# Performance work log

Hardware: AMD Instinct MI355X
Metric: run time of the kernel (lower is better)

The kernel has to match this reference:

```python
import jax, jax.numpy as jnp
import numpy as np

B = 8
H_IN, W_IN = 448, 448
STRIDE = 32
NUM_CLASSES = 20
CONF_THRESH = 0.01
NMS_THRESH = 0.5
HS, WS = H_IN // STRIDE, W_IN // STRIDE  # 14, 14
N_CELLS = HS * WS  # 196
CHANNELS = [3, 64, 128, 256, 512, 512]
HEAD_OUT = 1 + NUM_CLASSES + 4  # 25


def _conv(x, w, stride):
    return jax.lax.conv_general_dilated(
        x, w, (stride, stride), 'SAME',
        dimension_numbers=('NCHW', 'OIHW', 'NCHW'))


def _create_grid():
    gy, gx = jnp.meshgrid(jnp.arange(HS), jnp.arange(WS), indexing='ij')
    return jnp.stack([gx, gy], -1).reshape(1, N_CELLS, 2).astype(jnp.float32)


def _iou_matrix(boxes):
    # boxes: [N,4] xyxy -> [N,N] pairwise IoU
    x1, y1, x2, y2 = boxes[:, 0], boxes[:, 1], boxes[:, 2], boxes[:, 3]
    area = jnp.maximum(x2 - x1, 0.0) * jnp.maximum(y2 - y1, 0.0)
    ix1 = jnp.maximum(x1[:, None], x1[None, :])
    iy1 = jnp.maximum(y1[:, None], y1[None, :])
    ix2 = jnp.minimum(x2[:, None], x2[None, :])
    iy2 = jnp.minimum(y2[:, None], y2[None, :])
    inter = jnp.maximum(ix2 - ix1, 0.0) * jnp.maximum(iy2 - iy1, 0.0)
    return inter / (area[:, None] + area[None, :] - inter + 1e-14)


def _nms_keep(scores, iou):
    # greedy per-class NMS; scores [N], iou [N,N] -> bool keep mask [N]
    order = jnp.argsort(-scores)
    iou_s = iou[order][:, order]
    idx = jnp.arange(N_CELLS)
    valid = scores[order] > CONF_THRESH

    def body(i, keep):
        sup = (iou_s[i] > NMS_THRESH) & (idx > i) & keep[i]
        return keep & (~sup)

    keep = jax.lax.fori_loop(0, N_CELLS, body, valid)
    return jnp.zeros(N_CELLS, bool).at[order].set(keep)


def setup_inputs() -> dict:
    key = jax.random.key(0)
    ks = jax.random.split(key, 8)
    x = jax.random.normal(ks[0], (B, 3, H_IN, W_IN), dtype=jnp.float32)
    params = {}
    for i in range(5):
        cin, cout = CHANNELS[i], CHANNELS[i + 1]
        std = np.sqrt(2.0 / (cin * 9))
        params[f'w{i+1}'] = jax.random.normal(ks[i + 1], (cout, cin, 3, 3), dtype=jnp.float32) * std
    std = np.sqrt(2.0 / CHANNELS[-1])
    params['w_head'] = jax.random.normal(ks[6], (HEAD_OUT, CHANNELS[-1], 1, 1), dtype=jnp.float32) * std
    return {'x': x, **params}


def reference(x, w1, w2, w3, w4, w5, w_head):
    # backbone: 5 stride-2 conv+relu stages -> stride 32
    h = x
    for w in (w1, w2, w3, w4, w5):
        h = jax.nn.relu(_conv(h, w, 2))
    pred = _conv(h, w_head, 1)                      # [B, 25, 14, 14]
    pred = pred.reshape(B, HEAD_OUT, N_CELLS).transpose(0, 2, 1)  # [B, N, 25]

    conf = jax.nn.sigmoid(pred[..., 0:1])                              # [B,N,1]
    cls_scores = jax.nn.softmax(pred[..., 1:1 + NUM_CLASSES], -1) * conf  # [B,N,C]
    txtytwth = pred[..., 1 + NUM_CLASSES:]                             # [B,N,4]

    grid = _create_grid()                                              # [1,N,2]
    xy = (jax.nn.sigmoid(txtytwth[..., :2]) + grid) * STRIDE
    wh = jnp.exp(txtytwth[..., 2:]) * STRIDE
    scale = jnp.array([W_IN, H_IN, W_IN, H_IN], dtype=jnp.float32)
    boxes = jnp.concatenate([xy - wh * 0.5, xy + wh * 0.5], -1) / scale
    boxes = jnp.clip(boxes, 0.0, 1.0)                                  # [B,N,4]

    iou = jax.vmap(_iou_matrix)(boxes)                                 # [B,N,N]
    # per-class NMS, vmapped over classes then batch
    nms_c = jax.vmap(_nms_keep, in_axes=(-1, None), out_axes=-1)       # [N,C]
    keep = jax.vmap(nms_c, in_axes=(0, 0))(cls_scores, iou)            # [B,N,C]
    final_scores = cls_scores * keep
    return jnp.concatenate([boxes, final_scores], -1)                  # [B,N,4+C]
```

## Files before the change

### kernel.cpp

```cpp
#include <hip/hip_runtime.h>
#include <math.h>

#define BATCH 8
#define NCELLS 196
#define NCLS 20
#define HEADC 25

typedef __attribute__((ext_vector_type(8))) short short8;
typedef __attribute__((ext_vector_type(4))) float f32x4;
#define MFMA16(a,b,c) __builtin_amdgcn_mfma_f32_16x16x32_bf16(a,b,c,0,0,0)

__device__ __forceinline__ unsigned short f2bf(float x) {
    union { float f; unsigned u; } a; a.f = x;
    unsigned r = a.u + 0x7FFFu + ((a.u >> 16) & 1u);
    return (unsigned short)(r >> 16);
}
__device__ __forceinline__ float bf2f(unsigned short h) {
    union { unsigned u; float f; } a; a.u = ((unsigned)h) << 16;
    return a.f;
}
__device__ __forceinline__ void split_bf(float x, unsigned short& h, unsigned short& l) {
    h = f2bf(x);
    l = f2bf(x - bf2f(h));
}

__device__ __forceinline__ void prep_one(const float* __restrict__ w, int CIN, int COUT,
                                         int idx, unsigned short* __restrict__ whi,
                                         unsigned short* __restrict__ wlo) {
    int G = COUT >> 4, CH = CIN >> 5;
    int j    = idx & 7;
    int lane = (idx >> 3) & 63;
    int fg   = idx >> 9;
    int g    = fg % G;
    int fc   = fg / G;
    int chunk = fc % CH;
    int plane = fc / CH;
    int co = g * 16 + (lane & 15);
    int ci = chunk * 32 + (lane >> 4) * 8 + j;
    int ky = plane / 3, kx = plane % 3;
    float v = w[((co * CIN + ci) * 3 + ky) * 3 + kx];
    unsigned short h, l; split_bf(v, h, l);
    whi[idx] = h; wlo[idx] = l;
}
__global__ void prep_all(const float* __restrict__ w2, const float* __restrict__ w3,
                         const float* __restrict__ w4, const float* __restrict__ w5,
                         unsigned short* __restrict__ w2h, unsigned short* __restrict__ w2l,
                         unsigned short* __restrict__ w3h, unsigned short* __restrict__ w3l,
                         unsigned short* __restrict__ w4h, unsigned short* __restrict__ w4l,
                         unsigned short* __restrict__ w5h, unsigned short* __restrict__ w5l) {
    int idx = blockIdx.x * 256 + threadIdx.x;
    const int n2 = 73728, n3 = 294912, n4 = 1179648, n5 = 2359296;
    if (idx < n2) { prep_one(w2, 64, 128, idx, w2h, w2l); return; }
    idx -= n2;
    if (idx < n3) { prep_one(w3, 128, 256, idx, w3h, w3l); return; }
    idx -= n3;
    if (idx < n4) { prep_one(w4, 256, 512, idx, w4h, w4l); return; }
    idx -= n4;
    if (idx < n5) { prep_one(w5, 512, 512, idx, w5h, w5l); }
}

__global__ void conv1_kernel(const float* __restrict__ x, const float* __restrict__ w1,
                             unsigned short* __restrict__ ohi, unsigned short* __restrict__ olo) {
    __shared__ float sW[27][64];
    __shared__ float sX[3][3][66];
    int bid = blockIdx.x;
    int xseg = bid % 7;  bid /= 7;
    int oy   = bid % 224;
    int b    = bid / 224;
    int ox0  = xseg * 32;

    for (int e = threadIdx.x; e < 1728; e += 256) {
        int k = e >> 6, co = e & 63;
        sW[k][co] = w1[co * 27 + k];
    }
    for (int e = threadIdx.x; e < 594; e += 256) {
        int ci = e / 198;
        int r  = e - ci * 198;
        int ky = r / 66;
        int lx = r - ky * 66;
        int iy = 2 * oy + ky;
        int ix = 2 * ox0 + lx;
        float v = 0.f;
        if (lx < 65 && iy < 448 && ix < 448)
            v = x[(((size_t)b * 3 + ci) * 448 + iy) * 448 + ix];
        sX[ci][ky][lx] = v;
    }
    __syncthreads();

    int pxl = threadIdx.x >> 3;
    int cog = threadIdx.x & 7;
    float acc[8] = {0.f,0.f,0.f,0.f,0.f,0.f,0.f,0.f};
    #pragma unroll
    for (int ci = 0; ci < 3; ci++) {
        #pragma unroll
        for (int ky = 0; ky < 3; ky++) {
            const float* row = sX[ci][ky];
            #pragma unroll
            for (int kx = 0; kx < 3; kx++) {
                float iv = row[2 * pxl + kx];
                int k = (ci * 3 + ky) * 3 + kx;
                float4 wa = *(const float4*)&sW[k][cog * 8];
                float4 wb = *(const float4*)&sW[k][cog * 8 + 4];
                acc[0] += wa.x * iv; acc[1] += wa.y * iv; acc[2] += wa.z * iv; acc[3] += wa.w * iv;
                acc[4] += wb.x * iv; acc[5] += wb.y * iv; acc[6] += wb.z * iv; acc[7] += wb.w * iv;
            }
        }
    }
    union { unsigned short u[8]; uint4 v; } ph, pl;
    #pragma unroll
    for (int u = 0; u < 8; u++) {
        float v = fmaxf(acc[u], 0.f);
        split_bf(v, ph.u[u], pl.u[u]);
    }
    size_t base = ((size_t)(b * 224 + oy) * 224 + ox0 + pxl) * 64 + cog * 8;
    *(uint4*)&ohi[base] = ph.v;
    *(uint4*)&olo[base] = pl.v;
}

template<int CIN, int COUT, int HIN, int WIN, int KSPLIT, bool PARTIAL>
__launch_bounds__(256, 4)
__global__ void conv_mfma(const unsigned short* __restrict__ ahi, const unsigned short* __restrict__ alo,
                          const unsigned short* __restrict__ whi, const unsigned short* __restrict__ wlo,
                          unsigned short* __restrict__ ohi, unsigned short* __restrict__ olo,
                          float* __restrict__ part) {
    constexpr int HOUT = HIN / 2, WOUT = WIN / 2;
    constexpr int TX = (WOUT + 7) / 8, TY = (HOUT + 7) / 8;
    constexpr int COG = COUT / 128;
    constexpr int CH_TOT = CIN / 32;
    constexpr int CH = CH_TOT / KSPLIT;
    constexpr int G = COUT / 16;
    constexpr int PLANE_E = 17 * 17 * 32;
    constexpr size_t PSZ = (size_t)BATCH * HOUT * WOUT * COUT;

    __shared__ __align__(16) unsigned short sA[2 * PLANE_E];

    int bid = blockIdx.x;
    int ks  = bid % KSPLIT; bid /= KSPLIT;
    int txi = bid % TX;     bid /= TX;
    int tyi = bid % TY;     bid /= TY;
    int cg  = bid % COG;
    int b   = bid / COG;
    int oy0 = tyi * 8, ox0 = txi * 8;
    int iy0 = oy0 * 2, ix0 = ox0 * 2;

    int tid = threadIdx.x;
    int w   = tid >> 6;
    int lane = tid & 63;
    int n = lane & 15, quad = lane >> 4;
    int cohalf = w & 1;
    int pxhalf = w >> 1;

    int oyl[2], oxl[2], pbase[2];
    #pragma unroll
    for (int t = 0; t < 2; t++) {
        int nt = pxhalf * 2 + t;
        int oy_off = (nt >> 1) * 4 + (n >> 2);
        int ox_off = (nt & 1) * 4 + (n & 3);
        oyl[t] = oy0 + oy_off;
        oxl[t] = ox0 + ox_off;
        pbase[t] = 2 * oy_off * 17 + 2 * ox_off;
    }

    f32x4 zero = {0.f, 0.f, 0.f, 0.f};
    f32x4 acc[4][2];
    #pragma unroll
    for (int g = 0; g < 4; g++)
        #pragma unroll
        for (int t = 0; t < 2; t++) acc[g][t] = zero;

    int g0 = cg * 8 + cohalf * 4;

    for (int ch = 0; ch < CH; ch++) {
        int chunk = ks * CH + ch;
        int ci0 = chunk * 32;
        __syncthreads();
        for (int e = tid; e < 17 * 17 * 8; e += 256) {
            int pxi = e >> 3, grp = e & 7;
            int liy = pxi / 17, lix = pxi - liy * 17;
            int iy = iy0 + liy, ix = ix0 + lix;
            uint4 v = make_uint4(0u, 0u, 0u, 0u);
            if (iy < HIN && ix < WIN) {
                const unsigned short* src = ((grp & 4) ? alo : ahi)
                    + ((size_t)(b * HIN + iy) * WIN + ix) * CIN + ci0 + (grp & 3) * 8;
                v = *(const uint4*)src;
            }
            int u = pxi * 4 + ((grp & 3) ^ ((pxi >> 1) & 3));
            *(uint4*)&sA[((grp >> 2) ? PLANE_E : 0) + u * 8] = v;
        }
        __syncthreads();
        #pragma unroll
        for (int pl = 0; pl < 9; pl++) {
            int ky = pl / 3, kx = pl % 3;
            size_t fbase = ((size_t)(pl * CH_TOT + chunk) * G + g0) * 512 + lane * 8;
            short8 Ah[4], Al[4];
            #pragma unroll
            for (int g = 0; g < 4; g++) {
                Ah[g] = *(const short8*)(whi + fbase + (size_t)g * 512);
                Al[g] = *(const short8*)(wlo + fbase + (size_t)g * 512);
            }
            int dp = ky * 17 + kx;
            short8 Bh[2], Bl[2];
            #pragma unroll
            for (int t = 0; t < 2; t++) {
                int p = pbase[t] + dp;
                int u = p * 4 + (quad ^ ((p >> 1) & 3));
                Bh[t] = *(const short8*)&sA[u * 8];
                Bl[t] = *(const short8*)&sA[PLANE_E + u * 8];
            }
            #pragma unroll
            for (int g = 0; g < 4; g++) {
                #pragma unroll
                for (int t = 0; t < 2; t++) {
                    acc[g][t] = MFMA16(Ah[g], Bh[t], acc[g][t]);
                    acc[g][t] = MFMA16(Ah[g], Bl[t], acc[g][t]);
                    acc[g][t] = MFMA16(Al[g], Bh[t], acc[g][t]);
                }
            }
        }
    }
    int cob = cg * 128 + cohalf * 64;
    #pragma unroll
    for (int g = 0; g < 4; g++) {
        #pragma unroll
        for (int t = 0; t < 2; t++) {
            if (oyl[t] >= HOUT || oxl[t] >= WOUT) continue;
            size_t base = ((size_t)(b * HOUT + oyl[t]) * WOUT + oxl[t]) * COUT
                          + cob + g * 16 + quad * 4;
            if (PARTIAL) {
                *(f32x4*)&part[(size_t)ks * PSZ + base] = acc[g][t];
            } else {
                unsigned long long h64 = 0ull, l64 = 0ull;
                #pragma unroll
                for (int r = 0; r < 4; r++) {
                    float v = fmaxf(acc[g][t][r], 0.f);
                    unsigned short hh, ll; split_bf(v, hh, ll);
                    h64 |= ((unsigned long long)hh) << (16 * r);
                    l64 |= ((unsigned long long)ll) << (16 * r);
                }
                *(unsigned long long*)&ohi[base] = h64;
                *(unsigned long long*)&olo[base] = l64;
            }
        }
    }
}

template<int KS>
__global__ void reduceN_split(const float* __restrict__ p, unsigned short* __restrict__ oh,
                              unsigned short* __restrict__ ol, int n) {
    int n4 = n >> 2;
    int i = blockIdx.x * 256 + threadIdx.x;
    if (i >= n4) return;
    const float4* p4 = (const float4*)p;
    float4 s = p4[i];
    #pragma unroll
    for (int k = 1; k < KS; k++) {
        float4 t = p4[i + (size_t)k * n4];
        s.x += t.x; s.y += t.y; s.z += t.z; s.w += t.w;
    }
    float v[4] = { fmaxf(s.x,0.f), fmaxf(s.y,0.f), fmaxf(s.z,0.f), fmaxf(s.w,0.f) };
    unsigned long long h64 = 0ull, l64 = 0ull;
    #pragma unroll
    for (int r = 0; r < 4; r++) {
        unsigned short hh, ll; split_bf(v[r], hh, ll);
        h64 |= ((unsigned long long)hh) << (16 * r);
        l64 |= ((unsigned long long)ll) << (16 * r);
    }
    *(unsigned long long*)&oh[i * 4] = h64;
    *(unsigned long long*)&ol[i * 4] = l64;
}

__global__ void head_decode_kernel(const unsigned short* __restrict__ ah,
                                   const unsigned short* __restrict__ al,
                                   const float* __restrict__ wh,
                                   float* __restrict__ out, float* __restrict__ cls) {
    int wave = threadIdx.x >> 6;
    int lane = threadIdx.x & 63;
    int cellid = blockIdx.x * 4 + wave;
    float acc[HEADC];
    #pragma unroll
    for (int c = 0; c < HEADC; c++) acc[c] = 0.f;
    for (int it = 0; it < 8; it++) {
        int ci = it * 64 + lane;
        size_t idx = (size_t)cellid * 512 + ci;
        float a = bf2f(ah[idx]) + bf2f(al[idx]);
        #pragma unroll
        for (int c = 0; c < HEADC; c++) acc[c] += a * wh[c * 512 + ci];
    }
    #pragma unroll
    for (int c = 0; c < HEADC; c++) {
        float v = acc[c];
        v += __shfl_down(v, 32); v += __shfl_down(v, 16); v += __shfl_down(v, 8);
        v += __shfl_down(v, 4);  v += __shfl_down(v, 2);  v += __shfl_down(v, 1);
        acc[c] = v;
    }
    if (lane == 0) {
        int cell = cellid % NCELLS;
        int gx = cell % 14, gy = cell / 14;
        float conf = 1.f / (1.f + expf(-acc[0]));
        float m = acc[1];
        #pragma unroll
        for (int c = 1; c < NCLS; c++) m = fmaxf(m, acc[1 + c]);
        float e[NCLS], s = 0.f;
        #pragma unroll
        for (int c = 0; c < NCLS; c++) { e[c] = expf(acc[1 + c] - m); s += e[c]; }
        float inv = conf / s;
        #pragma unroll
        for (int c = 0; c < NCLS; c++) cls[(size_t)cellid * NCLS + c] = e[c] * inv;
        float cx = (1.f / (1.f + expf(-acc[21])) + gx) * 32.f;
        float cy = (1.f / (1.f + expf(-acc[22])) + gy) * 32.f;
        float bw = expf(acc[23]) * 32.f;
        float bh = expf(acc[24]) * 32.f;
        float x1 = (cx - 0.5f * bw) / 448.f, y1 = (cy - 0.5f * bh) / 448.f;
        float x2 = (cx + 0.5f * bw) / 448.f, y2 = (cy + 0.5f * bh) / 448.f;
        x1 = fminf(fmaxf(x1, 0.f), 1.f); y1 = fminf(fmaxf(y1, 0.f), 1.f);
        x2 = fminf(fmaxf(x2, 0.f), 1.f); y2 = fminf(fmaxf(y2, 0.f), 1.f);
        float* o = out + (size_t)cellid * 24;
        o[0] = x1; o[1] = y1; o[2] = x2; o[3] = y2;
    }
}

__global__ void iou_kernel(const float* __restrict__ out, float* __restrict__ iou) {
    int idx = blockIdx.x * 256 + threadIdx.x;
    if (idx >= BATCH * NCELLS * NCELLS) return;
    int j = idx % NCELLS;
    int i = (idx / NCELLS) % NCELLS;
    int b = idx / (NCELLS * NCELLS);
    const float* bi = out + (((size_t)b * NCELLS) + i) * 24;
    const float* bj = out + (((size_t)b * NCELLS) + j) * 24;
    float ai = fmaxf(bi[2] - bi[0], 0.f) * fmaxf(bi[3] - bi[1], 0.f);
    float aj = fmaxf(bj[2] - bj[0], 0.f) * fmaxf(bj[3] - bj[1], 0.f);
    float ix1 = fmaxf(bi[0], bj[0]), iy1 = fmaxf(bi[1], bj[1]);
    float ix2 = fminf(bi[2], bj[2]), iy2 = fminf(bi[3], bj[3]);
    float inter = fmaxf(ix2 - ix1, 0.f) * fmaxf(iy2 - iy1, 0.f);
    iou[idx] = inter / (ai + aj - inter + 1e-14f);
}

__global__ void nms_kernel(const float* __restrict__ cls, const float* __restrict__ iou,
                           float* __restrict__ out) {
    int b = blockIdx.x / NCLS;
    int c = blockIdx.x % NCLS;
    __shared__ float sc[NCELLS];
    __shared__ float ssort[NCELLS];
    __shared__ int   ord[NCELLS];
    __shared__ __align__(16) unsigned long long smask[NCELLS][4];
    int j = threadIdx.x;
    int lane = j & 63;
    int w = j >> 6;
    float sj = 0.f;
    if (j < NCELLS) {
        sj = cls[(((size_t)b * NCELLS) + j) * NCLS + c];
        sc[j] = sj;
    }
    __syncthreads();
    if (j < NCELLS) {
        int r = 0;
        for (int k = 0; k < NCELLS; k++) {
            float sk = sc[k];
            r += (sk > sj) || (sk == sj && k < j);
        }
        ord[r] = j; ssort[r] = sj;
    }
    __syncthreads();
    const float* iob = iou + (size_t)b * NCELLS * NCELLS;
    int oc[4];
    #pragma unroll
    for (int k = 0; k < 4; k++) {
        int cidx = k * 64 + lane;
        oc[k] = (cidx < NCELLS) ? ord[cidx] : 0;
    }
    for (int i = w; i < NCELLS; i += 4) {
        const float* rowp = iob + ord[i] * NCELLS;
        #pragma unroll
        for (int k = 0; k < 4; k++) {
            int cidx = k * 64 + lane;
            bool sup = false;
            if (cidx < NCELLS && cidx > i)
                sup = rowp[oc[k]] > 0.5f;
            unsigned long long m = __ballot(sup);
            if (lane == 0) smask[i][k] = m;
        }
    }
    __syncthreads();
    unsigned long long keep[4];
    #pragma unroll
    for (int k = 0; k < 4; k++) {
        int cidx = k * 64 + lane;
        bool valid = (cidx < NCELLS) && (ssort[cidx] > 0.01f);
        keep[k] = __ballot(valid);
    }
    #pragma unroll
    for (int wi = 0; wi < 4; wi++) {
        int base = wi * 64;
        int lim = (NCELLS - base < 64) ? (NCELLS - base) : 64;
        for (int t = 0; t < lim; t++) {
            if ((keep[wi] >> t) & 1ull) {
                int i = base + t;
                keep[0] &= ~smask[i][0];
                keep[1] &= ~smask[i][1];
                keep[2] &= ~smask[i][2];
                keep[3] &= ~smask[i][3];
            }
        }
    }
    if (j < NCELLS) {
        bool kept = (keep[w] >> lane) & 1ull;
        out[(((size_t)b * NCELLS) + ord[j]) * 24 + 4 + c] = kept ? ssort[j] : 0.f;
    }
}

extern "C" void kernel_launch(void* const* d_in, const int* in_sizes, int n_in,
                              void* d_out, int out_size, void* d_ws, size_t ws_size,
                              hipStream_t stream) {
    const float* x  = (const float*)d_in[0];
    const float* w1 = (const float*)d_in[1];
    const float* w2 = (const float*)d_in[2];
    const float* w3 = (const float*)d_in[3];
    const float* w4 = (const float*)d_in[4];
    const float* w5 = (const float*)d_in[5];
    const float* wh = (const float*)d_in[6];
    float* out = (float*)d_out;
    char* base = (char*)d_ws;

    unsigned short* a1h = (unsigned short*)(base);
    unsigned short* a1l = a1h + 25690112;
    unsigned short* a3h = (unsigned short*)(base);
    unsigned short* a3l = a3h + 6422528;
    float* part4 = (float*)(base + 25690112);
    float* part5 = (float*)(base);
    unsigned short* a5h = (unsigned short*)(base + 51380224);
    unsigned short* a5l = a5h + 802816;
    float* clsb = (float*)(base + 54746240);
    float* ioub = (float*)(base + 54871680);
    unsigned short* a2h = (unsigned short*)(base + 102760448);
    unsigned short* a2l = a2h + 12845056;
    unsigned short* a4h = (unsigned short*)(base + 102760448);
    unsigned short* a4l = a4h + 3211264;
    unsigned short* w2h = (unsigned short*)(base + 154140672);
    unsigned short* w3h = w2h + 73728;
    unsigned short* w4h = w3h + 294912;
    unsigned short* w5h = w4h + 1179648;
    unsigned short* w2l = (unsigned short*)(base + 161955840);
    unsigned short* w3l = w2l + 73728;
    unsigned short* w4l = w3l + 294912;
    unsigned short* w5l = w4l + 1179648;

    prep_all<<<15264, 256, 0, stream>>>(w2, w3, w4, w5,
                                        w2h, w2l, w3h, w3l, w4h, w4l, w5h, w5l);

    conv1_kernel<<<12544, 256, 0, stream>>>(x, w1, a1h, a1l);

    conv_mfma<64, 128, 224, 224, 1, false><<<1568, 256, 0, stream>>>(
        a1h, a1l, w2h, w2l, a2h, a2l, nullptr);
    conv_mfma<128, 256, 112, 112, 1, false><<<784, 256, 0, stream>>>(
        a2h, a2l, w3h, w3l, a3h, a3l, nullptr);
    conv_mfma<256, 512, 56, 56, 2, true><<<1024, 256, 0, stream>>>(
        a3h, a3l, w4h, w4l, nullptr, nullptr, part4);
    reduceN_split<2><<<3136, 256, 0, stream>>>(part4, a4h, a4l, 3211264);
    conv_mfma<512, 512, 28, 28, 8, true><<<1024, 256, 0, stream>>>(
        a4h, a4l, w5h, w5l, nullptr, nullptr, part5);
    reduceN_split<8><<<784, 256, 0, stream>>>(part5, a5h, a5l, 802816);

    head_decode_kernel<<<392, 256, 0, stream>>>(a5h, a5l, wh, out, clsb);
    iou_kernel<<<1201, 256, 0, stream>>>(out, ioub);
    nms_kernel<<<160, 256, 0, stream>>>(clsb, ioub, out);
}
```

Baseline: 464.2 us.

## Double-buffer conv input tiles in LDS using async global-to-LDS loads

Replaces the synchronous register-staged copy of each 32-channel input chunk into shared memory with direct global-to-LDS loads (global_load_lds), double-buffered so the next chunk is fetched while MFMAs run on the current one. The swizzle moves to the source address side, and out-of-bounds slots are zero-filled with ordinary stores. Only one barrier per chunk remains instead of two. Shared memory per block doubles and launch bounds drop from 4 to 2 blocks per CU, which trades occupancy for overlap.

```diff
diff --git a/kernel.cpp b/kernel.cpp
--- a/kernel.cpp
+++ b/kernel.cpp
@@ -9,6 +9,10 @@
 typedef __attribute__((ext_vector_type(8))) short short8;
 typedef __attribute__((ext_vector_type(4))) float f32x4;
 #define MFMA16(a,b,c) __builtin_amdgcn_mfma_f32_16x16x32_bf16(a,b,c,0,0,0)
+
+#define GLOAD_LDS16(g, l) \
+    __builtin_amdgcn_global_load_lds((const __attribute__((address_space(1))) void*)(g), \
+                                     (__attribute__((address_space(3))) void*)(l), 16, 0, 0)
 
 __device__ __forceinline__ unsigned short f2bf(float x) {
     union { float f; unsigned u; } a; a.f = x;
@@ -118,7 +122,7 @@
 }
 
 template<int CIN, int COUT, int HIN, int WIN, int KSPLIT, bool PARTIAL>
-__launch_bounds__(256, 4)
+__launch_bounds__(256, 2)
 __global__ void conv_mfma(const unsigned short* __restrict__ ahi, const unsigned short* __restrict__ alo,
                           const unsigned short* __restrict__ whi, const unsigned short* __restrict__ wlo,
                           unsigned short* __restrict__ ohi, unsigned short* __restrict__ olo,
@@ -129,10 +133,10 @@
     constexpr int CH_TOT = CIN / 32;
     constexpr int CH = CH_TOT / KSPLIT;
     constexpr int G = COUT / 16;
-    constexpr int PLANE_E = 17 * 17 * 32;
+    constexpr int UNITS = 17 * 17 * 4;
     constexpr size_t PSZ = (size_t)BATCH * HOUT * WOUT * COUT;
 
-    __shared__ __align__(16) unsigned short sA[2 * PLANE_E];
+    __shared__ __align__(16) unsigned short sA[2][2][UNITS * 8];
 
     int bid = blockIdx.x;
     int ks  = bid % KSPLIT; bid /= KSPLIT;
@@ -170,27 +174,38 @@
 
     int g0 = cg * 8 + cohalf * 4;
 
+    auto stage = [&](int ch, int buf) {
+        int ci0 = (ks * CH + ch) * 32;
+        #pragma unroll
+        for (int m = 0; m < (UNITS + 255) / 256; m++) {
+            int e = m * 256 + tid;
+            if (e < UNITS) {
+                int pxi = e >> 2, gsl = e & 3;
+                int grp = gsl ^ ((pxi >> 1) & 3);
+                int liy = pxi / 17, lix = pxi - liy * 17;
+                int iy = iy0 + liy, ix = ix0 + lix;
+                if (iy < HIN && ix < WIN) {
+                    size_t off = ((size_t)(b * HIN + iy) * WIN + ix) * CIN + ci0 + grp * 8;
+                    int ebase = m * 256 + (tid & 192);
+                    GLOAD_LDS16(ahi + off, &sA[buf][0][ebase * 8]);
+                    GLOAD_LDS16(alo + off, &sA[buf][1][ebase * 8]);
+                } else {
+                    uint4 z = make_uint4(0u, 0u, 0u, 0u);
+                    *(uint4*)&sA[buf][0][e * 8] = z;
+                    *(uint4*)&sA[buf][1][e * 8] = z;
+                }
+            }
+        }
+    };
+
+    stage(0, 0);
+    int pb = 0;
     for (int ch = 0; ch < CH; ch++) {
+        __syncthreads();
+        if (ch + 1 < CH) stage(ch + 1, pb ^ 1);
         int chunk = ks * CH + ch;
-        int ci0 = chunk * 32;
-        __syncthreads();
-        for (int e = tid; e < 17 * 17 * 8; e += 256) {
-            int pxi = e >> 3, grp = e & 7;
-            int liy = pxi / 17, lix = pxi - liy * 17;
-            int iy = iy0 + liy, ix = ix0 + lix;
-            uint4 v = make_uint4(0u, 0u, 0u, 0u);
-            if (iy < HIN && ix < WIN) {
-                const unsigned short* src = ((grp & 4) ? alo : ahi)
-                    + ((size_t)(b * HIN + iy) * WIN + ix) * CIN + ci0 + (grp & 3) * 8;
-                v = *(const uint4*)src;
-            }
-            int u = pxi * 4 + ((grp & 3) ^ ((pxi >> 1) & 3));
-            *(uint4*)&sA[((grp >> 2) ? PLANE_E : 0) + u * 8] = v;
-        }
-        __syncthreads();
         #pragma unroll
         for (int pl = 0; pl < 9; pl++) {
-            int ky = pl / 3, kx = pl % 3;
             size_t fbase = ((size_t)(pl * CH_TOT + chunk) * G + g0) * 512 + lane * 8;
             short8 Ah[4], Al[4];
             #pragma unroll
@@ -198,14 +213,14 @@
                 Ah[g] = *(const short8*)(whi + fbase + (size_t)g * 512);
                 Al[g] = *(const short8*)(wlo + fbase + (size_t)g * 512);
             }
-            int dp = ky * 17 + kx;
+            int dp = (pl / 3) * 17 + (pl % 3);
             short8 Bh[2], Bl[2];
             #pragma unroll
             for (int t = 0; t < 2; t++) {
                 int p = pbase[t] + dp;
                 int u = p * 4 + (quad ^ ((p >> 1) & 3));
-                Bh[t] = *(const short8*)&sA[u * 8];
-                Bl[t] = *(const short8*)&sA[PLANE_E + u * 8];
+                Bh[t] = *(const short8*)&sA[pb][0][u * 8];
+                Bl[t] = *(const short8*)&sA[pb][1][u * 8];
             }
             #pragma unroll
             for (int g = 0; g < 4; g++) {
@@ -217,7 +232,9 @@
                 }
             }
         }
-    }
+        pb ^= 1;
+    }
+
     int cob = cg * 128 + cohalf * 64;
     #pragma unroll
     for (int g = 0; g < 4; g++) {
```

After: 487.8 us. +5.1%, slower.

## Retile conv MFMA warps with prefetched weights; fuse IoU into NMS

Applied to the files above, without the earlier changes.

The conv MFMA kernel now gives each warp 2 output-channel groups across all 4 pixel tiles, instead of 4 groups across 2 tiles. This changes the mix of weight loads and LDS activation loads per warp. It also adds a 3-slot register prefetch of weight fragments so global loads overlap the MFMAs. Separately, the standalone IoU kernel and its global N×N matrix are removed, and NMS computes IoU on the fly from boxes staged in shared memory. This saves a launch and the IoU matrix traffic but repeats the IoU arithmetic for every class block.

```diff
diff --git a/kernel.cpp b/kernel.cpp
--- a/kernel.cpp
+++ b/kernel.cpp
@@ -147,28 +147,26 @@
     int w   = tid >> 6;
     int lane = tid & 63;
     int n = lane & 15, quad = lane >> 4;
-    int cohalf = w & 1;
-    int pxhalf = w >> 1;
-
-    int oyl[2], oxl[2], pbase[2];
-    #pragma unroll
-    for (int t = 0; t < 2; t++) {
-        int nt = pxhalf * 2 + t;
-        int oy_off = (nt >> 1) * 4 + (n >> 2);
-        int ox_off = (nt & 1) * 4 + (n & 3);
-        oyl[t] = oy0 + oy_off;
-        oxl[t] = ox0 + ox_off;
-        pbase[t] = 2 * oy_off * 17 + 2 * ox_off;
+
+    int oyl[4], oxl[4], pbase[4];
+    #pragma unroll
+    for (int nt = 0; nt < 4; nt++) {
+        int oyq = nt >> 1, oxq = nt & 1;
+        int oy_off = oyq * 4 + (n >> 2);
+        int ox_off = oxq * 4 + (n & 3);
+        oyl[nt] = oy0 + oy_off;
+        oxl[nt] = ox0 + ox_off;
+        pbase[nt] = 2 * oy_off * 17 + 2 * ox_off;
     }
 
     f32x4 zero = {0.f, 0.f, 0.f, 0.f};
-    f32x4 acc[4][2];
-    #pragma unroll
-    for (int g = 0; g < 4; g++)
-        #pragma unroll
-        for (int t = 0; t < 2; t++) acc[g][t] = zero;
-
-    int g0 = cg * 8 + cohalf * 4;
+    f32x4 acc[2][4];
+    #pragma unroll
+    for (int ct = 0; ct < 2; ct++)
+        #pragma unroll
+        for (int nt = 0; nt < 4; nt++) acc[ct][nt] = zero;
+
+    int g0 = cg * 8 + w * 2;
 
     for (int ch = 0; ch < CH; ch++) {
         int chunk = ks * CH + ch;
@@ -188,51 +186,50 @@
             *(uint4*)&sA[((grp >> 2) ? PLANE_E : 0) + u * 8] = v;
         }
         __syncthreads();
+        short8 Ah[3][2], Al[3][2];
+        auto loadA = [&](int pl, int slot) {
+            size_t fbase = ((size_t)(pl * CH_TOT + chunk) * G + g0) * 512 + lane * 8;
+            Ah[slot][0] = *(const short8*)(whi + fbase);
+            Ah[slot][1] = *(const short8*)(whi + fbase + 512);
+            Al[slot][0] = *(const short8*)(wlo + fbase);
+            Al[slot][1] = *(const short8*)(wlo + fbase + 512);
+        };
+        loadA(0, 0); loadA(1, 1); loadA(2, 2);
         #pragma unroll
         for (int pl = 0; pl < 9; pl++) {
-            int ky = pl / 3, kx = pl % 3;
-            size_t fbase = ((size_t)(pl * CH_TOT + chunk) * G + g0) * 512 + lane * 8;
-            short8 Ah[4], Al[4];
+            const int slot = pl % 3;
+            int dp = (pl / 3) * 17 + (pl % 3);
             #pragma unroll
-            for (int g = 0; g < 4; g++) {
-                Ah[g] = *(const short8*)(whi + fbase + (size_t)g * 512);
-                Al[g] = *(const short8*)(wlo + fbase + (size_t)g * 512);
-            }
-            int dp = ky * 17 + kx;
-            short8 Bh[2], Bl[2];
-            #pragma unroll
-            for (int t = 0; t < 2; t++) {
-                int p = pbase[t] + dp;
+            for (int nt = 0; nt < 4; nt++) {
+                int p = pbase[nt] + dp;
                 int u = p * 4 + (quad ^ ((p >> 1) & 3));
-                Bh[t] = *(const short8*)&sA[u * 8];
-                Bl[t] = *(const short8*)&sA[PLANE_E + u * 8];
-            }
-            #pragma unroll
-            for (int g = 0; g < 4; g++) {
-                #pragma unroll
-                for (int t = 0; t < 2; t++) {
-                    acc[g][t] = MFMA16(Ah[g], Bh[t], acc[g][t]);
-                    acc[g][t] = MFMA16(Ah[g], Bl[t], acc[g][t]);
-                    acc[g][t] = MFMA16(Al[g], Bh[t], acc[g][t]);
-                }
-            }
-        }
-    }
-    int cob = cg * 128 + cohalf * 64;
-    #pragma unroll
-    for (int g = 0; g < 4; g++) {
-        #pragma unroll
-        for (int t = 0; t < 2; t++) {
-            if (oyl[t] >= HOUT || oxl[t] >= WOUT) continue;
-            size_t base = ((size_t)(b * HOUT + oyl[t]) * WOUT + oxl[t]) * COUT
-                          + cob + g * 16 + quad * 4;
+                short8 Bh = *(const short8*)&sA[u * 8];
+                short8 Bl = *(const short8*)&sA[PLANE_E + u * 8];
+                acc[0][nt] = MFMA16(Ah[slot][0], Bh, acc[0][nt]);
+                acc[0][nt] = MFMA16(Ah[slot][0], Bl, acc[0][nt]);
+                acc[0][nt] = MFMA16(Al[slot][0], Bh, acc[0][nt]);
+                acc[1][nt] = MFMA16(Ah[slot][1], Bh, acc[1][nt]);
+                acc[1][nt] = MFMA16(Ah[slot][1], Bl, acc[1][nt]);
+                acc[1][nt] = MFMA16(Al[slot][1], Bh, acc[1][nt]);
+            }
+            if (pl + 3 < 9) loadA(pl + 3, slot);
+        }
+    }
+    int cob = cg * 128 + w * 32;
+    #pragma unroll
+    for (int ct = 0; ct < 2; ct++) {
+        #pragma unroll
+        for (int nt = 0; nt < 4; nt++) {
+            if (oyl[nt] >= HOUT || oxl[nt] >= WOUT) continue;
+            size_t base = ((size_t)(b * HOUT + oyl[nt]) * WOUT + oxl[nt]) * COUT
+                          + cob + ct * 16 + quad * 4;
             if (PARTIAL) {
-                *(f32x4*)&part[(size_t)ks * PSZ + base] = acc[g][t];
+                *(f32x4*)&part[(size_t)ks * PSZ + base] = acc[ct][nt];
             } else {
                 unsigned long long h64 = 0ull, l64 = 0ull;
                 #pragma unroll
                 for (int r = 0; r < 4; r++) {
-                    float v = fmaxf(acc[g][t][r], 0.f);
+                    float v = fmaxf(acc[ct][nt][r], 0.f);
                     unsigned short hh, ll; split_bf(v, hh, ll);
                     h64 |= ((unsigned long long)hh) << (16 * r);
                     l64 |= ((unsigned long long)ll) << (16 * r);
@@ -319,29 +316,15 @@
     }
 }
 
-__global__ void iou_kernel(const float* __restrict__ out, float* __restrict__ iou) {
-    int idx = blockIdx.x * 256 + threadIdx.x;
-    if (idx >= BATCH * NCELLS * NCELLS) return;
-    int j = idx % NCELLS;
-    int i = (idx / NCELLS) % NCELLS;
-    int b = idx / (NCELLS * NCELLS);
-    const float* bi = out + (((size_t)b * NCELLS) + i) * 24;
-    const float* bj = out + (((size_t)b * NCELLS) + j) * 24;
-    float ai = fmaxf(bi[2] - bi[0], 0.f) * fmaxf(bi[3] - bi[1], 0.f);
-    float aj = fmaxf(bj[2] - bj[0], 0.f) * fmaxf(bj[3] - bj[1], 0.f);
-    float ix1 = fmaxf(bi[0], bj[0]), iy1 = fmaxf(bi[1], bj[1]);
-    float ix2 = fminf(bi[2], bj[2]), iy2 = fminf(bi[3], bj[3]);
-    float inter = fmaxf(ix2 - ix1, 0.f) * fmaxf(iy2 - iy1, 0.f);
-    iou[idx] = inter / (ai + aj - inter + 1e-14f);
-}
-
-__global__ void nms_kernel(const float* __restrict__ cls, const float* __restrict__ iou,
+__global__ void nms_kernel(const float* __restrict__ cls, const float* __restrict__ boxes,
                            float* __restrict__ out) {
     int b = blockIdx.x / NCLS;
     int c = blockIdx.x % NCLS;
     __shared__ float sc[NCELLS];
     __shared__ float ssort[NCELLS];
     __shared__ int   ord[NCELLS];
+    __shared__ __align__(16) float sbox[NCELLS][4];
+    __shared__ float sarea[NCELLS];
     __shared__ __align__(16) unsigned long long smask[NCELLS][4];
     int j = threadIdx.x;
     int lane = j & 63;
@@ -350,6 +333,9 @@
     if (j < NCELLS) {
         sj = cls[(((size_t)b * NCELLS) + j) * NCLS + c];
         sc[j] = sj;
+        float4 bx = *(const float4*)&boxes[(((size_t)b * NCELLS) + j) * 24];
+        *(float4*)sbox[j] = bx;
+        sarea[j] = fmaxf(bx.z - bx.x, 0.f) * fmaxf(bx.w - bx.y, 0.f);
     }
     __syncthreads();
     if (j < NCELLS) {
@@ -361,21 +347,31 @@
         ord[r] = j; ssort[r] = sj;
     }
     __syncthreads();
-    const float* iob = iou + (size_t)b * NCELLS * NCELLS;
-    int oc[4];
+    int oc[4]; float bx1[4], by1[4], bx2[4], by2[4], bar[4];
     #pragma unroll
     for (int k = 0; k < 4; k++) {
         int cidx = k * 64 + lane;
         oc[k] = (cidx < NCELLS) ? ord[cidx] : 0;
+        bx1[k] = sbox[oc[k]][0]; by1[k] = sbox[oc[k]][1];
+        bx2[k] = sbox[oc[k]][2]; by2[k] = sbox[oc[k]][3];
+        bar[k] = sarea[oc[k]];
     }
     for (int i = w; i < NCELLS; i += 4) {
-        const float* rowp = iob + ord[i] * NCELLS;
+        int oi = ord[i];
+        float ix1 = sbox[oi][0], iy1 = sbox[oi][1];
+        float ix2 = sbox[oi][2], iy2 = sbox[oi][3];
+        float ia  = sarea[oi];
         #pragma unroll
         for (int k = 0; k < 4; k++) {
             int cidx = k * 64 + lane;
             bool sup = false;
-            if (cidx < NCELLS && cidx > i)
-                sup = rowp[oc[k]] > 0.5f;
+            if (cidx < NCELLS && cidx > i) {
+                float xx1 = fmaxf(ix1, bx1[k]), yy1 = fmaxf(iy1, by1[k]);
+                float xx2 = fminf(ix2, bx2[k]), yy2 = fminf(iy2, by2[k]);
+                float inter = fmaxf(xx2 - xx1, 0.f) * fmaxf(yy2 - yy1, 0.f);
+                float iou = inter / (ia + bar[k] - inter + 1e-14f);
+                sup = iou > 0.5f;
+            }
             unsigned long long m = __ballot(sup);
             if (lane == 0) smask[i][k] = m;
         }
@@ -430,7 +426,6 @@
     unsigned short* a5h = (unsigned short*)(base + 51380224);
     unsigned short* a5l = a5h + 802816;
     float* clsb = (float*)(base + 54746240);
-    float* ioub = (float*)(base + 54871680);
     unsigned short* a2h = (unsigned short*)(base + 102760448);
     unsigned short* a2l = a2h + 12845056;
     unsigned short* a4h = (unsigned short*)(base + 102760448);
@@ -461,6 +456,5 @@
     reduceN_split<8><<<784, 256, 0, stream>>>(part5, a5h, a5l, 802816);
 
     head_decode_kernel<<<392, 256, 0, stream>>>(a5h, a5l, wh, out, clsb);
-    iou_kernel<<<1201, 256, 0, stream>>>(out, ioub);
-    nms_kernel<<<160, 256, 0, stream>>>(clsb, ioub, out);
-}
+    nms_kernel<<<160, 256, 0, stream>>>(clsb, out, out);
+}
```

After: 445.9 us. 3.9% less time.
